# Performance work log

Measured on AMD Instinct MI355X. Metric: run time of the kernel, lower is better.

The kernel has to match this reference:

```python
import jax, jax.numpy as jnp
import numpy as np

D_MODEL = 1024
NUM_HEADS = 16
D_K = D_MODEL // NUM_HEADS


def setup_inputs() -> dict:
    key = jax.random.key(0)
    ks = jax.random.split(key, 5)
    B, S = 4, 2048
    scale = 1.0 / np.sqrt(D_MODEL)
    x = jax.random.normal(ks[0], (B, S, D_MODEL), dtype=jnp.float32)
    # Linear(d_model, d_model, bias=False) weights, stored as [out, in] like torch
    Wq = jax.random.normal(ks[1], (D_MODEL, D_MODEL), dtype=jnp.float32) * scale
    Wk = jax.random.normal(ks[2], (D_MODEL, D_MODEL), dtype=jnp.float32) * scale
    Wv = jax.random.normal(ks[3], (D_MODEL, D_MODEL), dtype=jnp.float32) * scale
    Wo = jax.random.normal(ks[4], (D_MODEL, D_MODEL), dtype=jnp.float32) * scale
    return {"x": x, "Wq": Wq, "Wk": Wk, "Wv": Wv, "Wo": Wo}


def reference(x, Wq, Wk, Wv, Wo):
    B, S, D = x.shape
    H, dk = NUM_HEADS, D_K
    # projections (torch Linear: x @ W.T)
    q = (x @ Wq.T).reshape(B, S, H, dk).transpose(0, 2, 1, 3)  # [B,H,S,dk]
    k = (x @ Wk.T).reshape(B, S, H, dk).transpose(0, 2, 1, 3)
    v = (x @ Wv.T).reshape(B, S, H, dk).transpose(0, 2, 1, 3)
    scores = jnp.einsum("bhqd,bhkd->bhqk", q, k) / jnp.sqrt(jnp.float32(dk))
    causal = jnp.triu(jnp.ones((S, S), dtype=bool), k=1)  # True above diagonal -> masked
    scores = jnp.where(causal[None, None], -jnp.inf, scores)
    attn = jax.nn.softmax(scores, axis=-1)
    out = jnp.einsum("bhqk,bhkd->bhqd", attn, v)  # [B,H,S,dk]
    out = out.transpose(0, 2, 1, 3).reshape(B, S, D)
    return out @ Wo.T
```

## Files before the change

kernel.cpp:

```cpp
#include <hip/hip_runtime.h>

typedef __bf16 bf16_t;
typedef __bf16 bf16x8 __attribute__((ext_vector_type(8)));
typedef __bf16 bf16x4 __attribute__((ext_vector_type(4)));
typedef float f32x4 __attribute__((ext_vector_type(4)));
typedef unsigned short u16x8 __attribute__((ext_vector_type(8)));

#define AS1C(p) ((const __attribute__((address_space(1))) void*)(p))
#define AS3(p) ((__attribute__((address_space(3))) void*)(p))
#define MM(a, b, c) __builtin_amdgcn_mfma_f32_16x16x32_bf16(a, b, c, 0, 0, 0)

__device__ __forceinline__ unsigned short f2b_rne(float f) {
  union { float f; unsigned u; } x; x.f = f;
  unsigned u = x.u;
  u += 0x7fffu + ((u >> 16) & 1u);
  return (unsigned short)(u >> 16);
}

__device__ __forceinline__ float fast_exp2(float x) {
  return __builtin_amdgcn_exp2f(x);
}

__global__ __launch_bounds__(256) void cast_f32_bf16(const float* __restrict__ in,
                                                     unsigned short* __restrict__ out,
                                                     int n) {
  int i = (blockIdx.x * 256 + threadIdx.x) * 8;
  if (i >= n) return;
  const float4* p = reinterpret_cast<const float4*>(in + i);
  float4 a = p[0], b = p[1];
  u16x8 o;
  o[0] = f2b_rne(a.x); o[1] = f2b_rne(a.y); o[2] = f2b_rne(a.z); o[3] = f2b_rne(a.w);
  o[4] = f2b_rne(b.x); o[5] = f2b_rne(b.y); o[6] = f2b_rne(b.z); o[7] = f2b_rne(b.w);
  *reinterpret_cast<u16x8*>(out + i) = o;
}

__global__ __launch_bounds__(256) void cast_w4(const float* __restrict__ w0,
                                               const float* __restrict__ w1,
                                               const float* __restrict__ w2,
                                               const float* __restrict__ w3,
                                               unsigned short* __restrict__ out) {
  const float* in = (blockIdx.y == 0) ? w0 : (blockIdx.y == 1) ? w1
                  : (blockIdx.y == 2) ? w2 : w3;
  int i = (blockIdx.x * 256 + threadIdx.x) * 8;
  unsigned short* o = out + (size_t)blockIdx.y * (1024u * 1024u);
  const float4* p = reinterpret_cast<const float4*>(in + i);
  float4 a = p[0], b = p[1];
  u16x8 v;
  v[0] = f2b_rne(a.x); v[1] = f2b_rne(a.y); v[2] = f2b_rne(a.z); v[3] = f2b_rne(a.w);
  v[4] = f2b_rne(b.x); v[5] = f2b_rne(b.y); v[6] = f2b_rne(b.z); v[7] = f2b_rne(b.w);
  *reinterpret_cast<u16x8*>(o + i) = v;
}

template <int OUT_F32>
__global__ __launch_bounds__(512, 4) void gemmk(const bf16_t* __restrict__ A,
                                                const bf16_t* __restrict__ Bm,
                                                void* __restrict__ C,
                                                int M, int N, int K, int lda,
                                                float scale, int qlim) {
  extern __shared__ bf16_t lds[];
  const int tid = threadIdx.x;
  const int w = tid >> 6, l = tid & 63;
  const int r = l & 15, kg = l >> 4;
  const int wm = (w >> 2) * 64;
  const int wn = (w & 3) * 64;
  const int m0 = blockIdx.y * 128, n0 = blockIdx.x * 256;
  const int srow = w * 16 + (l >> 2);
  const int scol = (l & 3) * 8;
  const bf16_t* aS = A + (size_t)(m0 + srow) * lda + scol;
  const bf16_t* bS = Bm + (size_t)(n0 + srow) * K + scol;

  f32x4 acc[4][4] = {};

  auto STAGE = [&](bf16_t* sb, int kt) {
    __builtin_amdgcn_global_load_lds(AS1C(aS + kt * 32), AS3(sb + w * 512), 16, 0, 0);
    __builtin_amdgcn_global_load_lds(AS1C(bS + kt * 32), AS3(sb + 4096 + w * 512), 16, 0, 0);
    __builtin_amdgcn_global_load_lds(AS1C(bS + (size_t)128 * K + kt * 32),
                                     AS3(sb + 8192 + w * 512), 16, 0, 0);
  };

  bf16_t* cur = lds;
  bf16_t* nxt = lds + 12288;
  bf16_t* stg = lds + 24576;

  STAGE(cur, 0);
  STAGE(nxt, 1);
  asm volatile("s_waitcnt vmcnt(3)" ::: "memory");
  __builtin_amdgcn_s_barrier();

  const int NT = K >> 5;
  for (int t = 0; t < NT; ++t) {
    bf16x8 AF[4], BF[4];
#pragma unroll
    for (int il = 0; il < 4; ++il)
      AF[il] = *reinterpret_cast<const bf16x8*>(cur + (wm + il * 16 + r) * 32 + kg * 8);
#pragma unroll
    for (int jl = 0; jl < 4; ++jl)
      BF[jl] = *reinterpret_cast<const bf16x8*>(cur + 4096 + (wn + jl * 16 + r) * 32 + kg * 8);
    const int kt = (t + 2 < NT) ? t + 2 : t;
    STAGE(stg, kt);
    asm volatile("s_waitcnt lgkmcnt(2)" ::: "memory");
    __builtin_amdgcn_sched_barrier(0);
    __builtin_amdgcn_s_setprio(1);
#pragma unroll
    for (int il = 0; il < 4; ++il)
#pragma unroll
      for (int jl = 0; jl < 2; ++jl)
        acc[il][jl] = MM(AF[il], BF[jl], acc[il][jl]);
    __builtin_amdgcn_s_setprio(0);
    asm volatile("s_waitcnt lgkmcnt(0)" ::: "memory");
    __builtin_amdgcn_sched_barrier(0);
    __builtin_amdgcn_s_setprio(1);
#pragma unroll
    for (int il = 0; il < 4; ++il)
#pragma unroll
      for (int jl = 2; jl < 4; ++jl)
        acc[il][jl] = MM(AF[il], BF[jl], acc[il][jl]);
    __builtin_amdgcn_s_setprio(0);
    asm volatile("s_waitcnt vmcnt(3)" ::: "memory");
    __builtin_amdgcn_s_barrier();
    bf16_t* tmp = cur; cur = nxt; nxt = stg; stg = tmp;
  }

#pragma unroll
  for (int il = 0; il < 4; ++il)
#pragma unroll
    for (int jl = 0; jl < 4; ++jl) {
      const int row0 = m0 + wm + il * 16 + kg * 4;
      const int col = n0 + wn + jl * 16 + r;
      const float sc = (col < qlim) ? scale : 1.0f;
#pragma unroll
      for (int v = 0; v < 4; ++v) {
        float val = acc[il][jl][v] * sc;
        size_t idx = (size_t)(row0 + v) * N + col;
        if (OUT_F32) reinterpret_cast<float*>(C)[idx] = val;
        else reinterpret_cast<unsigned short*>(C)[idx] = f2b_rne(val);
      }
    }
}

__global__ __launch_bounds__(256) void transpose_v(const bf16_t* __restrict__ qkv,
                                                   bf16_t* __restrict__ vt) {
  __shared__ bf16_t Vs[64 * 72];
  const int t = threadIdx.x;
  const int s0 = blockIdx.x * 64;
  const int bh = blockIdx.y;
  const int b = bh >> 4, h = bh & 15;
  const size_t in_base = ((size_t)b * 2048 + s0) * 3072 + 2048 + h * 64;
#pragma unroll
  for (int c = 0; c < 2; ++c) {
    int chunk = c * 256 + t;
    int ss = chunk >> 3, dd = (chunk & 7) * 8;
    bf16x8 v = *reinterpret_cast<const bf16x8*>(qkv + in_base + (size_t)ss * 3072 + dd);
    *reinterpret_cast<bf16x8*>(Vs + ss * 72 + dd) = v;
  }
  __syncthreads();
  const size_t out_base = (size_t)bh * 64 * 2048 + s0;
#pragma unroll
  for (int c = 0; c < 2; ++c) {
    int chunk = c * 256 + t;
    int dd = chunk >> 3, ss = (chunk & 7) * 8;
    bf16x8 o;
#pragma unroll
    for (int j = 0; j < 8; ++j) o[j] = Vs[(ss + j) * 72 + dd];
    *reinterpret_cast<bf16x8*>(vt + out_base + (size_t)dd * 2048 + ss) = o;
  }
}

__global__ __launch_bounds__(512, 6) void flash_attn(const bf16_t* __restrict__ QKV,
                                                     const bf16_t* __restrict__ VT,
                                                     unsigned short* __restrict__ O,
                                                     int ostride) {
  __shared__ bf16_t Ks[2][64 * 72];
  __shared__ bf16_t Vts[2][64 * 72];
  __shared__ bf16_t Pl[8][16 * 68];
  const int tid = threadIdx.x;
  const int lane = tid & 63, wave = tid >> 6;
  const int r = lane & 15, kg = lane >> 4;
  const int bh = blockIdx.x;
  const int qt = 15 - (int)blockIdx.y;
  const int b = bh >> 4, h = bh & 15;
  const size_t qkv_row0 = (size_t)b * 2048 * 3072;
  const int qcol = h * 64, kcol = 1024 + h * 64;
  const size_t vt_base = (size_t)bh * 64 * 2048;
  const size_t o_row0 = (size_t)b * 2048 * ostride;
  const int ocol = h * 64;
  const int srr = tid >> 3, scc = (tid & 7) * 8;

  const int q0 = qt * 128;
  const int qrow = q0 + wave * 16 + r;
  const int tmax_w = (q0 + wave * 16 + 15) >> 6;
  const int ntiles = qt * 2 + 2;

  const size_t qoff = qkv_row0 + (size_t)qrow * 3072 + qcol;
  bf16x8 qf0 = *reinterpret_cast<const bf16x8*>(QKV + qoff + kg * 8);
  bf16x8 qf1 = *reinterpret_cast<const bf16x8*>(QKV + qoff + 32 + kg * 8);

  f32x4 oacc[4] = {};
  float m_run = -3e30f, l_lane = 0.f;

  bf16x8 gk = *reinterpret_cast<const bf16x8*>(QKV + qkv_row0 + (size_t)srr * 3072 + kcol + scc);
  bf16x8 gv = *reinterpret_cast<const bf16x8*>(VT + vt_base + (size_t)srr * 2048 + scc);

  for (int t = 0; t < ntiles; ++t) {
    const int buf = t & 1;
    *reinterpret_cast<bf16x8*>(&Ks[buf][srr * 72 + scc]) = gk;
    *reinterpret_cast<bf16x8*>(&Vts[buf][srr * 72 + scc]) = gv;
    __syncthreads();
    if (t + 1 < ntiles) {
      const int kv1 = (t + 1) * 64;
      gk = *reinterpret_cast<const bf16x8*>(QKV + qkv_row0 + (size_t)(kv1 + srr) * 3072 + kcol + scc);
      gv = *reinterpret_cast<const bf16x8*>(VT + vt_base + (size_t)srr * 2048 + kv1 + scc);
    }
    if (t > tmax_w) continue;

    const int kv0 = t * 64;
    float vals[16];
#pragma unroll
    for (int nt = 0; nt < 4; ++nt) {
      bf16x8 kf0 = *reinterpret_cast<const bf16x8*>(&Ks[buf][(nt * 16 + r) * 72 + kg * 8]);
      bf16x8 kf1 = *reinterpret_cast<const bf16x8*>(&Ks[buf][(nt * 16 + r) * 72 + 32 + kg * 8]);
      f32x4 s = {};
      __builtin_amdgcn_s_setprio(1);
      s = MM(kf0, qf0, s);
      s = MM(kf1, qf1, s);
      __builtin_amdgcn_s_setprio(0);
#pragma unroll
      for (int v = 0; v < 4; ++v) vals[nt * 4 + v] = s[v];
    }
    if (t == tmax_w) {
#pragma unroll
      for (int nt = 0; nt < 4; ++nt)
#pragma unroll
        for (int v = 0; v < 4; ++v)
          if (kv0 + nt * 16 + kg * 4 + v > qrow) vals[nt * 4 + v] = -3e30f;
    }
    float a0 = fmaxf(fmaxf(vals[0], vals[1]), vals[2]);
    float a1 = fmaxf(fmaxf(vals[3], vals[4]), vals[5]);
    float a2 = fmaxf(fmaxf(vals[6], vals[7]), vals[8]);
    float a3 = fmaxf(fmaxf(vals[9], vals[10]), vals[11]);
    float a4 = fmaxf(fmaxf(vals[12], vals[13]), vals[14]);
    float pmax = fmaxf(fmaxf(fmaxf(a0, a1), fmaxf(a2, a3)), fmaxf(a4, vals[15]));
    if (!__all(pmax <= m_run + 8.0f)) {
      pmax = fmaxf(pmax, __shfl_xor(pmax, 16));
      pmax = fmaxf(pmax, __shfl_xor(pmax, 32));
      const float m_new = fmaxf(m_run, pmax);
      const float alpha = fast_exp2(m_run - m_new);
      l_lane *= alpha;
      f32x4 al;
#pragma unroll
      for (int v = 0; v < 4; ++v) al[v] = __shfl(alpha, kg * 4 + v);
#pragma unroll
      for (int dt = 0; dt < 4; ++dt)
#pragma unroll
        for (int v = 0; v < 4; ++v) oacc[dt][v] *= al[v];
      m_run = m_new;
    }
#pragma unroll
    for (int ii = 0; ii < 16; ++ii) {
      float p = fast_exp2(vals[ii] - m_run);
      vals[ii] = p;
      l_lane += p;
    }
#pragma unroll
    for (int nt = 0; nt < 4; ++nt) {
      bf16x4 pb;
#pragma unroll
      for (int v = 0; v < 4; ++v) pb[v] = (bf16_t)vals[nt * 4 + v];
      *reinterpret_cast<bf16x4*>(&Pl[wave][r * 68 + nt * 16 + kg * 4]) = pb;
    }
    bf16x8 pa0 = *reinterpret_cast<const bf16x8*>(&Pl[wave][r * 68 + kg * 8]);
    bf16x8 pa1 = *reinterpret_cast<const bf16x8*>(&Pl[wave][r * 68 + 32 + kg * 8]);
#pragma unroll
    for (int dt = 0; dt < 4; ++dt) {
      bf16x8 vb0 = *reinterpret_cast<const bf16x8*>(&Vts[buf][(dt * 16 + r) * 72 + kg * 8]);
      bf16x8 vb1 = *reinterpret_cast<const bf16x8*>(&Vts[buf][(dt * 16 + r) * 72 + 32 + kg * 8]);
      __builtin_amdgcn_s_setprio(1);
      oacc[dt] = MM(pa0, vb0, oacc[dt]);
      oacc[dt] = MM(pa1, vb1, oacc[dt]);
      __builtin_amdgcn_s_setprio(0);
    }
  }

  float l_row = l_lane;
  l_row += __shfl_xor(l_row, 16);
  l_row += __shfl_xor(l_row, 32);
  const float linv = 1.0f / l_row;
  f32x4 il;
#pragma unroll
  for (int v = 0; v < 4; ++v) il[v] = __shfl(linv, kg * 4 + v);
  const size_t orow0 = o_row0 + (size_t)(q0 + wave * 16) * ostride + ocol;
#pragma unroll
  for (int dt = 0; dt < 4; ++dt) {
    const int d = dt * 16 + r;
#pragma unroll
    for (int v = 0; v < 4; ++v)
      O[orow0 + (size_t)(kg * 4 + v) * ostride + d] = f2b_rne(oacc[dt][v] * il[v]);
  }
}

extern "C" void kernel_launch(void* const* d_in, const int* in_sizes, int n_in,
                              void* d_out, int out_size, void* d_ws, size_t ws_size,
                              hipStream_t stream) {
  const float* x  = (const float*)d_in[0];
  const float* Wq = (const float*)d_in[1];
  const float* Wk = (const float*)d_in[2];
  const float* Wv = (const float*)d_in[3];
  const float* Wo = (const float*)d_in[4];

  char* ws = (char*)d_ws;
  bf16_t* xb  = (bf16_t*)(ws);
  bf16_t* wqb = (bf16_t*)(ws + (16u << 20));
  bf16_t* wob = (bf16_t*)(ws + (22u << 20));
  bf16_t* qkv = (bf16_t*)(ws + (24u << 20));
  bf16_t* vt  = (bf16_t*)(ws);

  hipFuncSetAttribute(reinterpret_cast<const void*>(&gemmk<0>),
                      hipFuncAttributeMaxDynamicSharedMemorySize, 73728);
  hipFuncSetAttribute(reinterpret_cast<const void*>(&gemmk<1>),
                      hipFuncAttributeMaxDynamicSharedMemorySize, 73728);

  const int NX = 4 * 2048 * 1024;
  cast_f32_bf16<<<NX / 2048, 256, 0, stream>>>(x, (unsigned short*)xb, NX);
  cast_w4<<<dim3(512, 4), 256, 0, stream>>>(Wq, Wk, Wv, Wo, (unsigned short*)wqb);

  gemmk<0><<<dim3(3072 / 256, 8192 / 128), 512, 73728, stream>>>(
      xb, wqb, qkv, 8192, 3072, 1024, 1024, 0.18033688011112042f, 1024);

  transpose_v<<<dim3(2048 / 64, 64), 256, 0, stream>>>(qkv, vt);

  flash_attn<<<dim3(64, 16), 512, 0, stream>>>(qkv, vt, (unsigned short*)qkv, 3072);

  gemmk<1><<<dim3(1024 / 256, 8192 / 128), 512, 73728, stream>>>(
      qkv, wob, d_out, 8192, 1024, 1024, 3072, 1.0f, 0);
}
```

Measured before the change: 180.9 us.

## Pair low and high causal query tiles per block to share K/V loads

Each attention block now processes two query tiles, a low one and its mirrored high one, so the causal work per block is balanced. K and V tiles loaded into shared memory are reused by both query tiles, roughly halving K/V traffic, and the grid shrinks from 16 to 8 blocks along y. The cost is twice the accumulator and score registers, which is why launch bounds drop from 6 to 4 waves per SIMD, so occupancy falls and register spills are possible.

```diff
diff --git a/kernel.cpp b/kernel.cpp
--- a/kernel.cpp
+++ b/kernel.cpp
@@ -166,18 +166,18 @@
   }
 }
 
-__global__ __launch_bounds__(512, 6) void flash_attn(const bf16_t* __restrict__ QKV,
+__global__ __launch_bounds__(512, 4) void flash_attn(const bf16_t* __restrict__ QKV,
                                                      const bf16_t* __restrict__ VT,
                                                      unsigned short* __restrict__ O,
                                                      int ostride) {
   __shared__ bf16_t Ks[2][64 * 72];
   __shared__ bf16_t Vts[2][64 * 72];
-  __shared__ bf16_t Pl[8][16 * 68];
+  __shared__ bf16_t Pl[8][2][16 * 68];
   const int tid = threadIdx.x;
   const int lane = tid & 63, wave = tid >> 6;
   const int r = lane & 15, kg = lane >> 4;
   const int bh = blockIdx.x;
-  const int qt = 15 - (int)blockIdx.y;
+  const int pair = blockIdx.y;
   const int b = bh >> 4, h = bh & 15;
   const size_t qkv_row0 = (size_t)b * 2048 * 3072;
   const int qcol = h * 64, kcol = 1024 + h * 64;
@@ -186,115 +186,203 @@
   const int ocol = h * 64;
   const int srr = tid >> 3, scc = (tid & 7) * 8;
 
-  const int q0 = qt * 128;
-  const int qrow = q0 + wave * 16 + r;
-  const int tmax_w = (q0 + wave * 16 + 15) >> 6;
-  const int ntiles = qt * 2 + 2;
-
-  const size_t qoff = qkv_row0 + (size_t)qrow * 3072 + qcol;
-  bf16x8 qf0 = *reinterpret_cast<const bf16x8*>(QKV + qoff + kg * 8);
-  bf16x8 qf1 = *reinterpret_cast<const bf16x8*>(QKV + qoff + 32 + kg * 8);
-
-  f32x4 oacc[4] = {};
-  float m_run = -3e30f, l_lane = 0.f;
+  const int q0L = pair * 128, q0H = (15 - pair) * 128;
+  const int qrowL = q0L + wave * 16 + r, qrowH = q0H + wave * 16 + r;
+  const int tmaxL = (q0L + wave * 16 + 15) >> 6;
+  const int tmaxH = (q0H + wave * 16 + 15) >> 6;
+  const int NT = 32 - 2 * pair;
+
+  const size_t qoffL = qkv_row0 + (size_t)qrowL * 3072 + qcol;
+  const size_t qoffH = qkv_row0 + (size_t)qrowH * 3072 + qcol;
+  bf16x8 qfL0 = *reinterpret_cast<const bf16x8*>(QKV + qoffL + kg * 8);
+  bf16x8 qfL1 = *reinterpret_cast<const bf16x8*>(QKV + qoffL + 32 + kg * 8);
+  bf16x8 qfH0 = *reinterpret_cast<const bf16x8*>(QKV + qoffH + kg * 8);
+  bf16x8 qfH1 = *reinterpret_cast<const bf16x8*>(QKV + qoffH + 32 + kg * 8);
+
+  f32x4 oaccL[4] = {}, oaccH[4] = {};
+  float mL = -3e30f, lL = 0.f, mH = -3e30f, lH = 0.f;
 
   bf16x8 gk = *reinterpret_cast<const bf16x8*>(QKV + qkv_row0 + (size_t)srr * 3072 + kcol + scc);
   bf16x8 gv = *reinterpret_cast<const bf16x8*>(VT + vt_base + (size_t)srr * 2048 + scc);
 
-  for (int t = 0; t < ntiles; ++t) {
+  for (int t = 0; t < NT; ++t) {
     const int buf = t & 1;
     *reinterpret_cast<bf16x8*>(&Ks[buf][srr * 72 + scc]) = gk;
     *reinterpret_cast<bf16x8*>(&Vts[buf][srr * 72 + scc]) = gv;
     __syncthreads();
-    if (t + 1 < ntiles) {
+    if (t + 1 < NT) {
       const int kv1 = (t + 1) * 64;
       gk = *reinterpret_cast<const bf16x8*>(QKV + qkv_row0 + (size_t)(kv1 + srr) * 3072 + kcol + scc);
       gv = *reinterpret_cast<const bf16x8*>(VT + vt_base + (size_t)srr * 2048 + kv1 + scc);
     }
-    if (t > tmax_w) continue;
+    if (t > tmaxH) continue;
 
     const int kv0 = t * 64;
-    float vals[16];
+    const bool doL = (t <= tmaxL);
+
+    float valsL[16], valsH[16];
+    __builtin_amdgcn_s_setprio(1);
 #pragma unroll
     for (int nt = 0; nt < 4; ++nt) {
       bf16x8 kf0 = *reinterpret_cast<const bf16x8*>(&Ks[buf][(nt * 16 + r) * 72 + kg * 8]);
       bf16x8 kf1 = *reinterpret_cast<const bf16x8*>(&Ks[buf][(nt * 16 + r) * 72 + 32 + kg * 8]);
-      f32x4 s = {};
+      f32x4 sH = {};
+      sH = MM(kf0, qfH0, sH);
+      sH = MM(kf1, qfH1, sH);
+#pragma unroll
+      for (int v = 0; v < 4; ++v) valsH[nt * 4 + v] = sH[v];
+      if (doL) {
+        f32x4 sL = {};
+        sL = MM(kf0, qfL0, sL);
+        sL = MM(kf1, qfL1, sL);
+#pragma unroll
+        for (int v = 0; v < 4; ++v) valsL[nt * 4 + v] = sL[v];
+      }
+    }
+    __builtin_amdgcn_s_setprio(0);
+
+    if (doL) {
+      if (t == tmaxL) {
+#pragma unroll
+        for (int nt = 0; nt < 4; ++nt)
+#pragma unroll
+          for (int v = 0; v < 4; ++v)
+            if (kv0 + nt * 16 + kg * 4 + v > qrowL) valsL[nt * 4 + v] = -3e30f;
+      }
+      float a0 = fmaxf(fmaxf(valsL[0], valsL[1]), valsL[2]);
+      float a1 = fmaxf(fmaxf(valsL[3], valsL[4]), valsL[5]);
+      float a2 = fmaxf(fmaxf(valsL[6], valsL[7]), valsL[8]);
+      float a3 = fmaxf(fmaxf(valsL[9], valsL[10]), valsL[11]);
+      float a4 = fmaxf(fmaxf(valsL[12], valsL[13]), valsL[14]);
+      float pmax = fmaxf(fmaxf(fmaxf(a0, a1), fmaxf(a2, a3)), fmaxf(a4, valsL[15]));
+      if (!__all(pmax <= mL + 8.0f)) {
+        pmax = fmaxf(pmax, __shfl_xor(pmax, 16));
+        pmax = fmaxf(pmax, __shfl_xor(pmax, 32));
+        const float m_new = fmaxf(mL, pmax);
+        const float alpha = fast_exp2(mL - m_new);
+        lL *= alpha;
+        f32x4 al;
+#pragma unroll
+        for (int v = 0; v < 4; ++v) al[v] = __shfl(alpha, kg * 4 + v);
+#pragma unroll
+        for (int dt = 0; dt < 4; ++dt)
+#pragma unroll
+          for (int v = 0; v < 4; ++v) oaccL[dt][v] *= al[v];
+        mL = m_new;
+      }
+#pragma unroll
+      for (int ii = 0; ii < 16; ++ii) {
+        float p = fast_exp2(valsL[ii] - mL);
+        valsL[ii] = p;
+        lL += p;
+      }
+#pragma unroll
+      for (int nt = 0; nt < 4; ++nt) {
+        bf16x4 pb;
+#pragma unroll
+        for (int v = 0; v < 4; ++v) pb[v] = (bf16_t)valsL[nt * 4 + v];
+        *reinterpret_cast<bf16x4*>(&Pl[wave][0][r * 68 + nt * 16 + kg * 4]) = pb;
+      }
+      bf16x8 pa0 = *reinterpret_cast<const bf16x8*>(&Pl[wave][0][r * 68 + kg * 8]);
+      bf16x8 pa1 = *reinterpret_cast<const bf16x8*>(&Pl[wave][0][r * 68 + 32 + kg * 8]);
+#pragma unroll
+      for (int dt = 0; dt < 4; ++dt) {
+        bf16x8 vb0 = *reinterpret_cast<const bf16x8*>(&Vts[buf][(dt * 16 + r) * 72 + kg * 8]);
+        bf16x8 vb1 = *reinterpret_cast<const bf16x8*>(&Vts[buf][(dt * 16 + r) * 72 + 32 + kg * 8]);
+        oaccL[dt] = MM(pa0, vb0, oaccL[dt]);
+        oaccL[dt] = MM(pa1, vb1, oaccL[dt]);
+      }
+    }
+
+    {
+      if (t == tmaxH) {
+#pragma unroll
+        for (int nt = 0; nt < 4; ++nt)
+#pragma unroll
+          for (int v = 0; v < 4; ++v)
+            if (kv0 + nt * 16 + kg * 4 + v > qrowH) valsH[nt * 4 + v] = -3e30f;
+      }
+      float a0 = fmaxf(fmaxf(valsH[0], valsH[1]), valsH[2]);
+      float a1 = fmaxf(fmaxf(valsH[3], valsH[4]), valsH[5]);
+      float a2 = fmaxf(fmaxf(valsH[6], valsH[7]), valsH[8]);
+      float a3 = fmaxf(fmaxf(valsH[9], valsH[10]), valsH[11]);
+      float a4 = fmaxf(fmaxf(valsH[12], valsH[13]), valsH[14]);
+      float pmax = fmaxf(fmaxf(fmaxf(a0, a1), fmaxf(a2, a3)), fmaxf(a4, valsH[15]));
+      if (!__all(pmax <= mH + 8.0f)) {
+        pmax = fmaxf(pmax, __shfl_xor(pmax, 16));
+        pmax = fmaxf(pmax, __shfl_xor(pmax, 32));
+        const float m_new = fmaxf(mH, pmax);
+        const float alpha = fast_exp2(mH - m_new);
+        lH *= alpha;
+        f32x4 al;
+#pragma unroll
+        for (int v = 0; v < 4; ++v) al[v] = __shfl(alpha, kg * 4 + v);
+#pragma unroll
+        for (int dt = 0; dt < 4; ++dt)
+#pragma unroll
+          for (int v = 0; v < 4; ++v) oaccH[dt][v] *= al[v];
+        mH = m_new;
+      }
+#pragma unroll
+      for (int ii = 0; ii < 16; ++ii) {
+        float p = fast_exp2(valsH[ii] - mH);
+        valsH[ii] = p;
+        lH += p;
+      }
+#pragma unroll
+      for (int nt = 0; nt < 4; ++nt) {
+        bf16x4 pb;
+#pragma unroll
+        for (int v = 0; v < 4; ++v) pb[v] = (bf16_t)valsH[nt * 4 + v];
+        *reinterpret_cast<bf16x4*>(&Pl[wave][1][r * 68 + nt * 16 + kg * 4]) = pb;
+      }
+      bf16x8 pa0 = *reinterpret_cast<const bf16x8*>(&Pl[wave][1][r * 68 + kg * 8]);
+      bf16x8 pa1 = *reinterpret_cast<const bf16x8*>(&Pl[wave][1][r * 68 + 32 + kg * 8]);
       __builtin_amdgcn_s_setprio(1);
-      s = MM(kf0, qf0, s);
-      s = MM(kf1, qf1, s);
+#pragma unroll
+      for (int dt = 0; dt < 4; ++dt) {
+        bf16x8 vb0 = *reinterpret_cast<const bf16x8*>(&Vts[buf][(dt * 16 + r) * 72 + kg * 8]);
+        bf16x8 vb1 = *reinterpret_cast<const bf16x8*>(&Vts[buf][(dt * 16 + r) * 72 + 32 + kg * 8]);
+        oaccH[dt] = MM(pa0, vb0, oaccH[dt]);
+        oaccH[dt] = MM(pa1, vb1, oaccH[dt]);
+      }
       __builtin_amdgcn_s_setprio(0);
-#pragma unroll
-      for (int v = 0; v < 4; ++v) vals[nt * 4 + v] = s[v];
-    }
-    if (t == tmax_w) {
-#pragma unroll
-      for (int nt = 0; nt < 4; ++nt)
-#pragma unroll
-        for (int v = 0; v < 4; ++v)
-          if (kv0 + nt * 16 + kg * 4 + v > qrow) vals[nt * 4 + v] = -3e30f;
-    }
-    float a0 = fmaxf(fmaxf(vals[0], vals[1]), vals[2]);
-    float a1 = fmaxf(fmaxf(vals[3], vals[4]), vals[5]);
-    float a2 = fmaxf(fmaxf(vals[6], vals[7]), vals[8]);
-    float a3 = fmaxf(fmaxf(vals[9], vals[10]), vals[11]);
-    float a4 = fmaxf(fmaxf(vals[12], vals[13]), vals[14]);
-    float pmax = fmaxf(fmaxf(fmaxf(a0, a1), fmaxf(a2, a3)), fmaxf(a4, vals[15]));
-    if (!__all(pmax <= m_run + 8.0f)) {
-      pmax = fmaxf(pmax, __shfl_xor(pmax, 16));
-      pmax = fmaxf(pmax, __shfl_xor(pmax, 32));
-      const float m_new = fmaxf(m_run, pmax);
-      const float alpha = fast_exp2(m_run - m_new);
-      l_lane *= alpha;
-      f32x4 al;
-#pragma unroll
-      for (int v = 0; v < 4; ++v) al[v] = __shfl(alpha, kg * 4 + v);
-#pragma unroll
-      for (int dt = 0; dt < 4; ++dt)
-#pragma unroll
-        for (int v = 0; v < 4; ++v) oacc[dt][v] *= al[v];
-      m_run = m_new;
-    }
-#pragma unroll
-    for (int ii = 0; ii < 16; ++ii) {
-      float p = fast_exp2(vals[ii] - m_run);
-      vals[ii] = p;
-      l_lane += p;
-    }
-#pragma unroll
-    for (int nt = 0; nt < 4; ++nt) {
-      bf16x4 pb;
-#pragma unroll
-      for (int v = 0; v < 4; ++v) pb[v] = (bf16_t)vals[nt * 4 + v];
-      *reinterpret_cast<bf16x4*>(&Pl[wave][r * 68 + nt * 16 + kg * 4]) = pb;
-    }
-    bf16x8 pa0 = *reinterpret_cast<const bf16x8*>(&Pl[wave][r * 68 + kg * 8]);
-    bf16x8 pa1 = *reinterpret_cast<const bf16x8*>(&Pl[wave][r * 68 + 32 + kg * 8]);
+    }
+  }
+
+  {
+    float l_row = lL;
+    l_row += __shfl_xor(l_row, 16);
+    l_row += __shfl_xor(l_row, 32);
+    const float linv = 1.0f / l_row;
+    f32x4 il;
+#pragma unroll
+    for (int v = 0; v < 4; ++v) il[v] = __shfl(linv, kg * 4 + v);
+    const size_t orow0 = o_row0 + (size_t)(q0L + wave * 16) * ostride + ocol;
 #pragma unroll
     for (int dt = 0; dt < 4; ++dt) {
-      bf16x8 vb0 = *reinterpret_cast<const bf16x8*>(&Vts[buf][(dt * 16 + r) * 72 + kg * 8]);
-      bf16x8 vb1 = *reinterpret_cast<const bf16x8*>(&Vts[buf][(dt * 16 + r) * 72 + 32 + kg * 8]);
-      __builtin_amdgcn_s_setprio(1);
-      oacc[dt] = MM(pa0, vb0, oacc[dt]);
-      oacc[dt] = MM(pa1, vb1, oacc[dt]);
-      __builtin_amdgcn_s_setprio(0);
-    }
-  }
-
-  float l_row = l_lane;
-  l_row += __shfl_xor(l_row, 16);
-  l_row += __shfl_xor(l_row, 32);
-  const float linv = 1.0f / l_row;
-  f32x4 il;
-#pragma unroll
-  for (int v = 0; v < 4; ++v) il[v] = __shfl(linv, kg * 4 + v);
-  const size_t orow0 = o_row0 + (size_t)(q0 + wave * 16) * ostride + ocol;
-#pragma unroll
-  for (int dt = 0; dt < 4; ++dt) {
-    const int d = dt * 16 + r;
-#pragma unroll
-    for (int v = 0; v < 4; ++v)
-      O[orow0 + (size_t)(kg * 4 + v) * ostride + d] = f2b_rne(oacc[dt][v] * il[v]);
+      const int d = dt * 16 + r;
+#pragma unroll
+      for (int v = 0; v < 4; ++v)
+        O[orow0 + (size_t)(kg * 4 + v) * ostride + d] = f2b_rne(oaccL[dt][v] * il[v]);
+    }
+  }
+  {
+    float l_row = lH;
+    l_row += __shfl_xor(l_row, 16);
+    l_row += __shfl_xor(l_row, 32);
+    const float linv = 1.0f / l_row;
+    f32x4 il;
+#pragma unroll
+    for (int v = 0; v < 4; ++v) il[v] = __shfl(linv, kg * 4 + v);
+    const size_t orow0 = o_row0 + (size_t)(q0H + wave * 16) * ostride + ocol;
+#pragma unroll
+    for (int dt = 0; dt < 4; ++dt) {
+      const int d = dt * 16 + r;
+#pragma unroll
+      for (int v = 0; v < 4; ++v)
+        O[orow0 + (size_t)(kg * 4 + v) * ostride + d] = f2b_rne(oaccH[dt][v] * il[v]);
+    }
   }
 }
 
@@ -328,7 +416,7 @@
 
   transpose_v<<<dim3(2048 / 64, 64), 256, 0, stream>>>(qkv, vt);
 
-  flash_attn<<<dim3(64, 16), 512, 0, stream>>>(qkv, vt, (unsigned short*)qkv, 3072);
+  flash_attn<<<dim3(64, 8), 512, 0, stream>>>(qkv, vt, (unsigned short*)qkv, 3072);
 
   gemmk<1><<<dim3(1024 / 256, 8192 / 128), 512, 73728, stream>>>(
       qkv, wob, d_out, 8192, 1024, 1024, 3072, 1.0f, 0);
```

New measurement: 172.5 us. 4.7% less time.
